# Kernel optimization log

Hardware: AMD Instinct MI355X
Metric: run time of the kernel (lower is better)

Reference implementation:

```python
import jax, jax.numpy as jnp
import numpy as np

D_MODEL = 1024
N_HEADS = 16
D_K = D_MODEL // N_HEADS


def setup_inputs() -> dict:
    key = jax.random.key(0)
    k1, k2, k3 = jax.random.split(key, 3)
    x = jax.random.normal(k1, (2, 2048, D_MODEL), dtype=jnp.float32)
    # torch Linear(d, 3d).weight has shape [3d, d]; y = x @ W.T
    W_qkv = jax.random.normal(k2, (3 * D_MODEL, D_MODEL), dtype=jnp.float32) * (1.0 / np.sqrt(D_MODEL))
    W_out = jax.random.normal(k3, (D_MODEL, D_MODEL), dtype=jnp.float32) * (1.0 / np.sqrt(D_MODEL))
    return {"x": x, "W_qkv": W_qkv, "W_out": W_out}


def reference(x, W_qkv, W_out):
    batch, seq_len, d_model = x.shape
    qkv = jnp.einsum('bsd,ed->bse', x, W_qkv)  # [b, s, 3*d_model]
    qkv = qkv.reshape(batch, seq_len, 3, N_HEADS, D_K)
    qkv = jnp.transpose(qkv, (2, 0, 3, 1, 4))  # [3, b, h, s, dk]
    Q, K, V = qkv[0], qkv[1], qkv[2]
    scale = 1.0 / jnp.sqrt(jnp.asarray(D_K, dtype=x.dtype))
    scores = jnp.einsum('bhqd,bhkd->bhqk', Q, K) * scale  # [b, h, s, s]
    causal = jnp.tril(jnp.ones((seq_len, seq_len), dtype=bool))
    scores = jnp.where(causal, scores, jnp.asarray(-jnp.inf, dtype=scores.dtype))
    attn = jax.nn.softmax(scores, axis=-1)
    out = jnp.einsum('bhqk,bhkd->bhqd', attn, V)  # [b, h, s, dk]
    out = jnp.transpose(out, (0, 2, 1, 3)).reshape(batch, seq_len, d_model)
    return jnp.einsum('bsd,ed->bse', out, W_out)
```

## Files before the change

### kernel.cpp

```cpp
#include <hip/hip_runtime.h>
#include <stdint.h>

#define DMODEL 1024
#define NHEADS 16
#define DKH 64
#define BATCH 2
#define SEQ 2048
#define MTOT (BATCH*SEQ)

typedef __bf16 bf16x8 __attribute__((ext_vector_type(8)));
typedef __bf16 bf16x4 __attribute__((ext_vector_type(4)));
typedef float  f32x4  __attribute__((ext_vector_type(4)));

__device__ __forceinline__ f32x4 mfma16(bf16x8 a, bf16x8 b, f32x4 c){
  return __builtin_amdgcn_mfma_f32_16x16x32_bf16(a, b, c, 0, 0, 0);
}

__device__ __forceinline__ void gload_lds16(const void* g, void* l){
  __builtin_amdgcn_global_load_lds(
      (const __attribute__((address_space(1))) uint32_t*)(uintptr_t)g,
      (__attribute__((address_space(3))) uint32_t*)(uint32_t)(uintptr_t)l,
      16, 0, 0);
}

__device__ __forceinline__ unsigned short f2bf(float f){
  unsigned u = __builtin_bit_cast(unsigned, f);
  u += 0x7fff + ((u >> 16) & 1);
  return (unsigned short)(u >> 16);
}

#define QSCALE 0.1803368801111372f

__global__ void cvt_kernel(const float* __restrict__ in, unsigned short* __restrict__ out, int n4){
  const float4*  in4  = (const float4*)in;
  ushort4*       out4 = (ushort4*)out;
  int i = blockIdx.x * blockDim.x + threadIdx.x;
  int stride = gridDim.x * blockDim.x;
  for (; i < n4; i += stride){
    float4 v = in4[i];
    ushort4 o;
    o.x = f2bf(v.x); o.y = f2bf(v.y); o.z = f2bf(v.z); o.w = f2bf(v.w);
    out4[i] = o;
  }
}

template<int EPI, int BM, int BN>
__global__ __launch_bounds__(256)
void gemm_bt(const __bf16* __restrict__ Ag, const __bf16* __restrict__ Bg,
             int M, int N, int K,
             __bf16* __restrict__ Qo, __bf16* __restrict__ Ko, __bf16* __restrict__ Vt,
             float* __restrict__ Co){
  constexpr int AM = BM/32;
  constexpr int AN = BN/32;
  constexpr int CA = BM/64;
  constexpr int CB = BN/64;
  __shared__ __align__(16) __bf16 As[2][BM*32];
  __shared__ __align__(16) __bf16 Bs[2][BN*32];
  const int tid  = threadIdx.x;
  const int wave = tid >> 6, lane = tid & 63;
  const int wr = wave >> 1, wc = wave & 1;
  const int lr = lane & 15, lg = lane >> 4;
  const int m0 = blockIdx.y * BM, n0 = blockIdx.x * BN;

  f32x4 acc[AM][AN] = {};

  const int srow = lane >> 2;
  const int scol = (lane & 3) * 8;
  const __bf16* gA = Ag + (size_t)(m0 + wave*(BM/4) + srow) * K + scol;
  const __bf16* gB = Bg + (size_t)(n0 + wave*(BN/4) + srow) * K + scol;

  const int nk = K >> 5;

#pragma unroll
  for (int c = 0; c < CA; c++)
    gload_lds16(gA + (size_t)(c*16)*K, &As[0][(wave*(BM/4) + c*16)*32]);
#pragma unroll
  for (int c = 0; c < CB; c++)
    gload_lds16(gB + (size_t)(c*16)*K, &Bs[0][(wave*(BN/4) + c*16)*32]);

  for (int t = 0; t < nk; t++){
    __syncthreads();
    if (t + 1 < nk){
      const int k0 = (t+1) << 5, b = (t+1) & 1;
#pragma unroll
      for (int c = 0; c < CA; c++)
        gload_lds16(gA + k0 + (size_t)(c*16)*K, &As[b][(wave*(BM/4) + c*16)*32]);
#pragma unroll
      for (int c = 0; c < CB; c++)
        gload_lds16(gB + k0 + (size_t)(c*16)*K, &Bs[b][(wave*(BN/4) + c*16)*32]);
    }
    const int cb = t & 1;
    bf16x8 af[AM], bfv[AN];
#pragma unroll
    for (int i = 0; i < AM; i++)
      af[i] = *(const bf16x8*)&As[cb][(wr*(BM/2) + i*16 + lr)*32 + lg*8];
#pragma unroll
    for (int j = 0; j < AN; j++)
      bfv[j] = *(const bf16x8*)&Bs[cb][(wc*(BN/2) + j*16 + lr)*32 + lg*8];
#pragma unroll
    for (int i = 0; i < AM; i++)
#pragma unroll
      for (int j = 0; j < AN; j++)
        acc[i][j] = mfma16(af[i], bfv[j], acc[i][j]);
  }

  if (EPI == 0){
    const int three = n0 >> 10;
#pragma unroll
    for (int i = 0; i < AM; i++){
#pragma unroll
      for (int j = 0; j < AN; j++){
#pragma unroll
        for (int r = 0; r < 4; r++){
          int m = m0 + wr*(BM/2) + i*16 + lg*4 + r;
          int n = n0 + wc*(BN/2) + j*16 + lr;
          int b = m >> 11, s = m & 2047;
          int h = (n >> 6) & 15, dk = n & 63;
          if (three == 0)      Qo[(((size_t)(b*NHEADS + h))*SEQ + s)*DKH + dk] = (__bf16)(acc[i][j][r] * QSCALE);
          else if (three == 1) Ko[(((size_t)(b*NHEADS + h))*SEQ + s)*DKH + dk] = (__bf16)acc[i][j][r];
          else                 Vt[(((size_t)(b*NHEADS + h))*DKH + dk)*SEQ + s] = (__bf16)acc[i][j][r];
        }
      }
    }
  } else {
#pragma unroll
    for (int i = 0; i < AM; i++)
#pragma unroll
      for (int j = 0; j < AN; j++)
#pragma unroll
        for (int r = 0; r < 4; r++){
          int m = m0 + wr*(BM/2) + i*16 + lg*4 + r;
          int n = n0 + wc*(BN/2) + j*16 + lr;
          Co[(size_t)m * N + n] = acc[i][j][r];
        }
  }
}

__global__ __launch_bounds__(128)
void attn_kernel(const __bf16* __restrict__ Q, const __bf16* __restrict__ K,
                 const __bf16* __restrict__ Vt, __bf16* __restrict__ Aout){
  const int id   = blockIdx.x;
  const int xcd  = id & 7;
  const int slot = id >> 3;
  const int bh   = (xcd << 2) | (slot >> 5);
  const int j    = slot & 31;
  const int wave = threadIdx.x >> 6, lane = threadIdx.x & 63;
  const int lr = lane & 15, lg = lane >> 4;
  const int swz = (lr & 7) << 4;

  const __bf16* Qh = Q + (size_t)bh*SEQ*DKH;
  const char* Kc = (const char*)(K  + (size_t)bh*SEQ*DKH);
  const char* Vc = (const char*)(Vt + (size_t)bh*DKH*SEQ);

  __shared__ __align__(16) char lds[2][16384];

  const int row8 = lane >> 3;
  const int cG   = ((lane & 7) << 4) ^ (row8 << 4);

  const int b = bh >> 4, h = bh & 15;

  for (int ph = 0; ph < 2; ph++){
    const int tb  = ph ? (63 - j) : j;
    const int qw  = tb*32 + wave*16;
    const int nkv = (tb >> 1) + 1;

    bf16x8 qf0 = *(const bf16x8*)(Qh + (size_t)(qw + lr)*DKH + lg*8);
    bf16x8 qf1 = *(const bf16x8*)(Qh + (size_t)(qw + lr)*DKH + 32 + lg*8);

    f32x4 o[4] = {};
    float mrun = -1e30f, lrun = 0.f;

#pragma unroll
    for (int i = 0; i < 4; i++){
      const int srow = wave*32 + i*8 + row8;
      gload_lds16(Kc + (size_t)srow*128 + cG,  &lds[0][wave*4096 + i*1024]);
      gload_lds16(Vc + (size_t)srow*4096 + cG, &lds[0][8192 + wave*4096 + i*1024]);
    }
    __syncthreads();

    for (int kb = 0; kb < nkv; kb++){
      const int kv0 = kb*64;
      if (kb + 1 < nkv){
        const int nv0 = kv0 + 64;
#pragma unroll
        for (int i = 0; i < 4; i++){
          const int srow = wave*32 + i*8 + row8;
          gload_lds16(Kc + (size_t)(nv0 + srow)*128 + cG,
                      &lds[(kb+1)&1][wave*4096 + i*1024]);
          gload_lds16(Vc + (size_t)srow*4096 + (size_t)nv0*2 + cG,
                      &lds[(kb+1)&1][8192 + wave*4096 + i*1024]);
        }
      }
      const char* Ks = lds[kb&1];
      const char* Vs = lds[kb&1] + 8192;

      f32x4 sf[4];
      __builtin_amdgcn_s_setprio(1);
#pragma unroll
      for (int t = 0; t < 4; t++){
        const int row = t*16 + lr;
        bf16x8 kf0 = *(const bf16x8*)(Ks + row*128 + ((lg*16) ^ swz));
        bf16x8 kf1 = *(const bf16x8*)(Ks + row*128 + ((64 + lg*16) ^ swz));
        f32x4 c = {};
        c = mfma16(kf0, qf0, c);
        c = mfma16(kf1, qf1, c);
        sf[t] = c;
      }
      __builtin_amdgcn_s_setprio(0);
      if (kv0 + 63 > qw){
        const int q = qw + lr;
#pragma unroll
        for (int t = 0; t < 4; t++)
#pragma unroll
          for (int r = 0; r < 4; r++){
            int kv = kv0 + t*16 + lg*4 + r;
            sf[t][r] = (kv <= q) ? sf[t][r] : -1e30f;
          }
      }
      float mx = fmaxf(fmaxf(fmaxf(sf[0][0], sf[0][1]), fmaxf(sf[0][2], sf[0][3])),
                       fmaxf(fmaxf(sf[1][0], sf[1][1]), fmaxf(sf[1][2], sf[1][3])));
      float mx2 = fmaxf(fmaxf(fmaxf(sf[2][0], sf[2][1]), fmaxf(sf[2][2], sf[2][3])),
                        fmaxf(fmaxf(sf[3][0], sf[3][1]), fmaxf(sf[3][2], sf[3][3])));
      mx = fmaxf(mx, mx2);
      mx = fmaxf(mx, __shfl_xor(mx, 16));
      mx = fmaxf(mx, __shfl_xor(mx, 32));

      if (!__all(mx <= mrun + 8.0f)){
        float mn = fmaxf(mrun, mx);
        float alpha = __builtin_amdgcn_exp2f(mrun - mn);
        mrun = mn;
        lrun *= alpha;
        float av[4];
#pragma unroll
        for (int r = 0; r < 4; r++) av[r] = __shfl(alpha, lg*4 + r);
#pragma unroll
        for (int n = 0; n < 4; n++)
#pragma unroll
          for (int r = 0; r < 4; r++) o[n][r] *= av[r];
      }

      float p[16];
#pragma unroll
      for (int t = 0; t < 4; t++)
#pragma unroll
        for (int r = 0; r < 4; r++){
          float v = __builtin_amdgcn_exp2f(sf[t][r] - mrun);
          p[t*4 + r] = v;
          lrun += v;
        }

      bf16x8 pa0, pa1;
#pragma unroll
      for (int i = 0; i < 8; i++){ pa0[i] = (__bf16)p[i]; pa1[i] = (__bf16)p[8 + i]; }
      __builtin_amdgcn_s_setprio(1);
#pragma unroll
      for (int n = 0; n < 4; n++){
        const int row = n*16 + lr;
        bf16x4 vlo0 = *(const bf16x4*)(Vs + row*128 + ((lg*8) ^ swz));
        bf16x4 vhi0 = *(const bf16x4*)(Vs + row*128 + ((32 + lg*8) ^ swz));
        bf16x4 vlo1 = *(const bf16x4*)(Vs + row*128 + ((64 + lg*8) ^ swz));
        bf16x4 vhi1 = *(const bf16x4*)(Vs + row*128 + ((96 + lg*8) ^ swz));
        bf16x8 vf0 = __builtin_shufflevector(vlo0, vhi0, 0,1,2,3,4,5,6,7);
        bf16x8 vf1 = __builtin_shufflevector(vlo1, vhi1, 0,1,2,3,4,5,6,7);
        o[n] = mfma16(pa0, vf0, o[n]);
        o[n] = mfma16(pa1, vf1, o[n]);
      }
      __builtin_amdgcn_s_setprio(0);
      __syncthreads();
    }

    lrun += __shfl_xor(lrun, 16);
    lrun += __shfl_xor(lrun, 32);
    float inv = 1.0f / lrun;
#pragma unroll
    for (int r = 0; r < 4; r++){
      float invr = __shfl(inv, lg*4 + r);
      __bf16* dst = Aout + ((size_t)b*SEQ + qw + lg*4 + r)*DMODEL + h*DKH;
#pragma unroll
      for (int n = 0; n < 4; n++)
        dst[n*16 + lr] = (__bf16)(o[n][r] * invr);
    }
  }
}

extern "C" void kernel_launch(void* const* d_in, const int* in_sizes, int n_in,
                              void* d_out, int out_size, void* d_ws, size_t ws_size,
                              hipStream_t stream){
  const float* x    = (const float*)d_in[0];
  const float* wqkv = (const float*)d_in[1];
  const float* wout = (const float*)d_in[2];
  float* out = (float*)d_out;
  char* ws = (char*)d_ws;

  __bf16* xb  = (__bf16*)(ws);
  __bf16* Ab  = (__bf16*)(ws);
  __bf16* wqb = (__bf16*)(ws + 8388608);
  __bf16* wob = (__bf16*)(ws + 14680064);
  __bf16* Qb  = (__bf16*)(ws + 16777216);
  __bf16* Kb  = (__bf16*)(ws + 25165824);
  __bf16* Vtb = (__bf16*)(ws + 33554432);

  cvt_kernel<<<1024, 256, 0, stream>>>(x,    (unsigned short*)xb,  (MTOT*DMODEL)/4);
  cvt_kernel<<<1024, 256, 0, stream>>>(wqkv, (unsigned short*)wqb, (3*DMODEL*DMODEL)/4);
  cvt_kernel<<<256,  256, 0, stream>>>(wout, (unsigned short*)wob, (DMODEL*DMODEL)/4);

  gemm_bt<0,128,128><<<dim3(24, 32), 256, 0, stream>>>(xb, wqb, MTOT, 3*DMODEL, DMODEL,
                                                       Qb, Kb, Vtb, nullptr);
  attn_kernel<<<1024, 128, 0, stream>>>(Qb, Kb, Vtb, Ab);
  gemm_bt<1,128,64><<<dim3(16, 32), 256, 0, stream>>>(Ab, wob, MTOT, DMODEL, DMODEL,
                                                      nullptr, nullptr, nullptr, out);
}
```

Baseline: 184.4 us.

## Fuse conversions, remap GEMM blocks per XCD, and coalesce V-transpose stores via LDS

The three fp32-to-bf16 conversion launches become a single kernel that walks one concatenated index range. The GEMM grid is flattened into a 1D launch and remapped so that consecutive blocks on the same XCD share row tiles, which should improve L2 reuse of A. The V-transpose epilogue now stages the tile through LDS and writes 16-byte contiguous runs along the sequence dimension, replacing the previous scattered 2-byte strided stores. The cost is extra barriers in the V epilogue and some index-computation overhead.

```diff
diff --git a/kernel.cpp b/kernel.cpp
--- a/kernel.cpp
+++ b/kernel.cpp
@@ -31,20 +31,27 @@
 
 #define QSCALE 0.1803368801111372f
 
-__global__ void cvt_kernel(const float* __restrict__ in, unsigned short* __restrict__ out, int n4){
-  const float4*  in4  = (const float4*)in;
-  ushort4*       out4 = (ushort4*)out;
+__global__ void cvt3_kernel(const float* __restrict__ a, const float* __restrict__ b,
+                            const float* __restrict__ c,
+                            unsigned short* __restrict__ oa, unsigned short* __restrict__ ob,
+                            unsigned short* __restrict__ oc,
+                            int na4, int nb4, int nc4){
   int i = blockIdx.x * blockDim.x + threadIdx.x;
-  int stride = gridDim.x * blockDim.x;
-  for (; i < n4; i += stride){
-    float4 v = in4[i];
+  const int tot = na4 + nb4 + nc4;
+  const int stride = gridDim.x * blockDim.x;
+  for (; i < tot; i += stride){
+    const float4* s; ushort4* d; int k;
+    if (i < na4)            { s = (const float4*)a; d = (ushort4*)oa; k = i; }
+    else if (i < na4 + nb4) { s = (const float4*)b; d = (ushort4*)ob; k = i - na4; }
+    else                    { s = (const float4*)c; d = (ushort4*)oc; k = i - na4 - nb4; }
+    float4 v = s[k];
     ushort4 o;
     o.x = f2bf(v.x); o.y = f2bf(v.y); o.z = f2bf(v.z); o.w = f2bf(v.w);
-    out4[i] = o;
+    d[k] = o;
   }
 }
 
-template<int EPI, int BM, int BN>
+template<int EPI, int BM, int BN, int NBN>
 __global__ __launch_bounds__(256)
 void gemm_bt(const __bf16* __restrict__ Ag, const __bf16* __restrict__ Bg,
              int M, int N, int K,
@@ -60,7 +67,12 @@
   const int wave = tid >> 6, lane = tid & 63;
   const int wr = wave >> 1, wc = wave & 1;
   const int lr = lane & 15, lg = lane >> 4;
-  const int m0 = blockIdx.y * BM, n0 = blockIdx.x * BN;
+
+  const int id  = blockIdx.x;
+  const int xcd = id & 7;
+  const int idx = id >> 3;
+  const int m0  = (xcd*4 + idx/NBN) * BM;
+  const int n0  = (idx % NBN) * BN;
 
   f32x4 acc[AM][AN] = {};
 
@@ -81,13 +93,13 @@
   for (int t = 0; t < nk; t++){
     __syncthreads();
     if (t + 1 < nk){
-      const int k0 = (t+1) << 5, b = (t+1) & 1;
+      const int k0 = (t+1) << 5, bb = (t+1) & 1;
 #pragma unroll
       for (int c = 0; c < CA; c++)
-        gload_lds16(gA + k0 + (size_t)(c*16)*K, &As[b][(wave*(BM/4) + c*16)*32]);
+        gload_lds16(gA + k0 + (size_t)(c*16)*K, &As[bb][(wave*(BM/4) + c*16)*32]);
 #pragma unroll
       for (int c = 0; c < CB; c++)
-        gload_lds16(gB + k0 + (size_t)(c*16)*K, &Bs[b][(wave*(BN/4) + c*16)*32]);
+        gload_lds16(gB + k0 + (size_t)(c*16)*K, &Bs[bb][(wave*(BN/4) + c*16)*32]);
     }
     const int cb = t & 1;
     bf16x8 af[AM], bfv[AN];
@@ -106,20 +118,46 @@
 
   if (EPI == 0){
     const int three = n0 >> 10;
-#pragma unroll
-    for (int i = 0; i < AM; i++){
+    if (three < 2){
+#pragma unroll
+      for (int i = 0; i < AM; i++){
+#pragma unroll
+        for (int j = 0; j < AN; j++){
+#pragma unroll
+          for (int r = 0; r < 4; r++){
+            int m = m0 + wr*(BM/2) + i*16 + lg*4 + r;
+            int n = n0 + wc*(BN/2) + j*16 + lr;
+            int b = m >> 11, s = m & 2047;
+            int h = (n >> 6) & 15, dk = n & 63;
+            if (three == 0) Qo[(((size_t)(b*NHEADS + h))*SEQ + s)*DKH + dk] = (__bf16)(acc[i][j][r] * QSCALE);
+            else            Ko[(((size_t)(b*NHEADS + h))*SEQ + s)*DKH + dk] = (__bf16)acc[i][j][r];
+          }
+        }
+      }
+    } else {
+      __bf16 (*T)[136] = (__bf16(*)[136])&As[0][0];
+      const int lrow = tid >> 3;
+      const int mc   = (tid & 7) * 16;
+      const int ngr  = (n0 - 2048) + ((lrow >> 4) << 6) + (lrow & 15);
+      const int bb   = m0 >> 11;
+      const int sbase= (m0 & 2047) + mc;
 #pragma unroll
       for (int j = 0; j < AN; j++){
-#pragma unroll
-        for (int r = 0; r < 4; r++){
-          int m = m0 + wr*(BM/2) + i*16 + lg*4 + r;
-          int n = n0 + wc*(BN/2) + j*16 + lr;
-          int b = m >> 11, s = m & 2047;
-          int h = (n >> 6) & 15, dk = n & 63;
-          if (three == 0)      Qo[(((size_t)(b*NHEADS + h))*SEQ + s)*DKH + dk] = (__bf16)(acc[i][j][r] * QSCALE);
-          else if (three == 1) Ko[(((size_t)(b*NHEADS + h))*SEQ + s)*DKH + dk] = (__bf16)acc[i][j][r];
-          else                 Vt[(((size_t)(b*NHEADS + h))*DKH + dk)*SEQ + s] = (__bf16)acc[i][j][r];
-        }
+        __syncthreads();
+#pragma unroll
+        for (int i = 0; i < AM; i++){
+          bf16x4 v;
+#pragma unroll
+          for (int r = 0; r < 4; r++) v[r] = (__bf16)acc[i][j][r];
+          *(bf16x4*)&T[wc*16 + lr][wr*64 + i*16 + lg*4] = v;
+        }
+        __syncthreads();
+        const int ng = ngr + j*16;
+        __bf16* dst = Vt + (((size_t)(bb*NHEADS) + (ng >> 6))*DKH + (ng & 63))*SEQ + sbase;
+        bf16x8 x0 = *(const bf16x8*)&T[lrow][mc];
+        bf16x8 x1 = *(const bf16x8*)&T[lrow][mc + 8];
+        *(bf16x8*)dst = x0;
+        *(bf16x8*)(dst + 8) = x1;
       }
     }
   } else {
@@ -300,13 +338,13 @@
   __bf16* Kb  = (__bf16*)(ws + 25165824);
   __bf16* Vtb = (__bf16*)(ws + 33554432);
 
-  cvt_kernel<<<1024, 256, 0, stream>>>(x,    (unsigned short*)xb,  (MTOT*DMODEL)/4);
-  cvt_kernel<<<1024, 256, 0, stream>>>(wqkv, (unsigned short*)wqb, (3*DMODEL*DMODEL)/4);
-  cvt_kernel<<<256,  256, 0, stream>>>(wout, (unsigned short*)wob, (DMODEL*DMODEL)/4);
-
-  gemm_bt<0,128,128><<<dim3(24, 32), 256, 0, stream>>>(xb, wqb, MTOT, 3*DMODEL, DMODEL,
-                                                       Qb, Kb, Vtb, nullptr);
+  cvt3_kernel<<<2048, 256, 0, stream>>>(x, wqkv, wout,
+                                        (unsigned short*)xb, (unsigned short*)wqb, (unsigned short*)wob,
+                                        (MTOT*DMODEL)/4, (3*DMODEL*DMODEL)/4, (DMODEL*DMODEL)/4);
+
+  gemm_bt<0,128,128,24><<<768, 256, 0, stream>>>(xb, wqb, MTOT, 3*DMODEL, DMODEL,
+                                                 Qb, Kb, Vtb, nullptr);
   attn_kernel<<<1024, 128, 0, stream>>>(Qb, Kb, Vtb, Ab);
-  gemm_bt<1,128,64><<<dim3(16, 32), 256, 0, stream>>>(Ab, wob, MTOT, DMODEL, DMODEL,
-                                                      nullptr, nullptr, nullptr, out);
-}
+  gemm_bt<1,128,64,16><<<512, 256, 0, stream>>>(Ab, wob, MTOT, DMODEL, DMODEL,
+                                                nullptr, nullptr, nullptr, out);
+}
```

After: 173.0 us. 1.07x faster.
